# Kernel tuning notes

Measured on AMD Instinct MI355X. Metric: run time of the kernel, lower is better.

## Reference

```python
import jax, jax.numpy as jnp
import numpy as np

B, N, E, H = 32, 256, 768, 12
D = E // H
SCALING = D ** -0.5


def setup_inputs() -> dict:
    key = jax.random.key(0)
    ks = jax.random.split(key, 10)
    inp = {
        "query": jax.random.normal(ks[0], (B, N, E), dtype=jnp.float32),
        "attn_bias": jax.random.normal(ks[1], (B * H, N, N), dtype=jnp.float32),
        "delta_pos": jax.random.normal(ks[2], (B, N, N, 3), dtype=jnp.float32),
        # Linear params stored as (in, out) so y = x @ W + b (equivalent to torch Linear).
        "Wq": jax.random.normal(ks[3], (E, E), dtype=jnp.float32) * 0.02,
        "bq": jnp.zeros((E,), dtype=jnp.float32),
        "Wk": jax.random.normal(ks[4], (E, E), dtype=jnp.float32) * 0.02,
        "bk": jnp.zeros((E,), dtype=jnp.float32),
        "Wv": jax.random.normal(ks[5], (E, E), dtype=jnp.float32) * 0.02,
        "bv": jnp.zeros((E,), dtype=jnp.float32),
        # force_proj: Linear(E, 1, bias=False) -> weight vector (E,)
        "wf": jax.random.normal(ks[6], (E,), dtype=jnp.float32) * 0.02,
    }
    return inp


def reference(query, attn_bias, delta_pos, Wq, bq, Wk, bk, Wv, bv, wf):
    b, n, e = query.shape
    h, d = H, D
    # QKV projections -> (b, n, h, d)
    q = (query @ Wq + bq).reshape(b, n, h, d) * SCALING
    k = (query @ Wk + bk).reshape(b, n, h, d)
    v = (query @ Wv + bv).reshape(b, n, h, d)
    # attention scores (b, h, n, n)
    attn = jnp.einsum("bnhd,bmhd->bhnm", q, k)
    # add bias on flattened (b*h, n, n), softmax over last dim (dropout=0.1 disabled: eval mode)
    probs = jax.nn.softmax(attn.reshape(b * h, n, n) + attn_bias, axis=-1)
    probs = probs.reshape(b, h, n, n)
    # equivariant weighted sum: x[b,n,c,h,d] = sum_m probs[b,h,n,m] * delta_pos[b,n,m,c] * v[b,m,h,d]
    x = jnp.einsum("bhnm,bnmc,bmhd->bnchd", probs, delta_pos, v)
    x = x.reshape(b, n, 3, e)
    # force projection (shared Linear(E,1,bias=False) applied per spatial component)
    force = jnp.einsum("bnce,e->bnc", x, wf).astype(jnp.float32)
    return force
```

## Files before the change

### kernel.cpp

```cpp
#include <hip/hip_runtime.h>
#include <hip/hip_bf16.h>

#define Bc 32
#define Nc 256
#define Ec 768
#define Hc 12
#define Dc 64

typedef __attribute__((ext_vector_type(8))) __bf16 bf16x8;
typedef __attribute__((ext_vector_type(8))) unsigned short u16x8;
typedef __attribute__((ext_vector_type(4))) float f32x4;

__device__ __forceinline__ unsigned short f2bf(float x) {
  union { float f; unsigned u; } v; v.f = x;
  unsigned r = v.u + 0x7fff + ((v.u >> 16) & 1);
  return (unsigned short)(r >> 16);
}

#define GL2LDS(gp, lp) __builtin_amdgcn_global_load_lds( \
    (__attribute__((address_space(1))) void*)(gp),        \
    (__attribute__((address_space(3))) void*)(lp), 16, 0, 0)

__global__ __launch_bounds__(256) void k_trans(const float* __restrict__ Wq,
                                               const float* __restrict__ Wk,
                                               unsigned short* __restrict__ WT) {
  __shared__ float tile[32][33];
  const float* W = blockIdx.z ? Wk : Wq;
  float scale = blockIdx.z ? 1.0f : 0.125f;
  int rowoff = blockIdx.z ? Ec : 0;
  int k0 = blockIdx.x * 32, n0 = blockIdx.y * 32;
  int r = threadIdx.x >> 5, c = threadIdx.x & 31;
  #pragma unroll
  for (int it = 0; it < 4; ++it)
    tile[r + 8 * it][c] = W[(k0 + r + 8 * it) * Ec + n0 + c];
  __syncthreads();
  #pragma unroll
  for (int it = 0; it < 4; ++it)
    WT[(rowoff + n0 + r + 8 * it) * Ec + k0 + c] = f2bf(scale * tile[c][r + 8 * it]);
}

__global__ void k_build_wvf(const float* __restrict__ Wv, const float* __restrict__ bv,
                            const float* __restrict__ wf,
                            const float* __restrict__ bq, const float* __restrict__ bk,
                            float* __restrict__ Wvf, float* __restrict__ bvf,
                            float* __restrict__ bb) {
  int idx = blockIdx.x * 256 + threadIdx.x;
  if (idx < Ec * Hc) {
    int e = idx / Hc, h = idx % Hc;
    float s = 0.f;
    for (int d = 0; d < Dc; ++d) s += Wv[e * Ec + h * Dc + d] * wf[h * Dc + d];
    Wvf[idx] = s;
  }
  if (idx < Hc) {
    float s = 0.f;
    for (int d = 0; d < Dc; ++d) s += bv[idx * Dc + d] * wf[idx * Dc + d];
    bvf[idx] = s;
  }
  if (idx < 2 * Ec)
    bb[idx] = (idx < Ec) ? 0.125f * bq[idx] : bk[idx - Ec];
}

__global__ __launch_bounds__(256) void k_vf(const float* __restrict__ query,
                                            const float* __restrict__ Wvf,
                                            const float* __restrict__ bvf,
                                            float* __restrict__ vfT,
                                            unsigned short* __restrict__ Xb) {
  __shared__ float wl[Ec * 13];
  __shared__ float bl[Hc];
  for (int i = threadIdx.x; i < Ec * Hc; i += 256) {
    int e = i / Hc, h = i % Hc;
    wl[e * 13 + h] = Wvf[i];
  }
  if (threadIdx.x < Hc) bl[threadIdx.x] = bvf[threadIdx.x];
  __syncthreads();
  int warp = threadIdx.x >> 6, lane = threadIdx.x & 63;
  int r = blockIdx.x * 4 + warp;
  float q[12];
  #pragma unroll
  for (int i = 0; i < 12; ++i) q[i] = query[r * Ec + lane + 64 * i];
  #pragma unroll
  for (int i = 0; i < 12; ++i) Xb[r * Ec + lane + 64 * i] = f2bf(q[i]);
  int b = r >> 8, m = r & 255;
  for (int h = 0; h < Hc; ++h) {
    float s = 0.f;
    #pragma unroll
    for (int i = 0; i < 12; ++i) s += q[i] * wl[(lane + 64 * i) * 13 + h];
    #pragma unroll
    for (int off = 32; off; off >>= 1) s += __shfl_xor(s, off);
    if (lane == 0) vfT[(b * Hc + h) * Nc + m] = s + bl[h];
  }
}

__global__ __launch_bounds__(256) void k_gemm_qk(const unsigned short* __restrict__ Xb,
                                                 const unsigned short* __restrict__ WT,
                                                 const float* __restrict__ bb,
                                                 unsigned short* __restrict__ QK) {
  __shared__ unsigned short As[128 * 64];
  __shared__ unsigned short Bs[128 * 64];
  int bm = blockIdx.x, bn = blockIdx.y;
  int t = threadIdx.x;
  int wave = t >> 6, lane = t & 63;
  int wr = wave >> 1, wc = wave & 1;
  int lrow = lane & 15, lq = lane >> 4;
  const int row0 = bm * 128, col0 = bn * 128;

  int srow = wave * 8 + (lane >> 3);
  int soct = (lane & 7);

  f32x4 acc[4][4];
  #pragma unroll
  for (int m = 0; m < 4; ++m)
    #pragma unroll
    for (int n = 0; n < 4; ++n) acc[m][n] = f32x4{0.f, 0.f, 0.f, 0.f};

  for (int ks = 0; ks < Ec; ks += 64) {
    #pragma unroll
    for (int i = 0; i < 4; ++i) {
      int r = i * 32 + srow;
      int go = soct ^ (r & 7);
      GL2LDS(Xb + (row0 + r) * Ec + ks + go * 8, As + i * 2048 + wave * 512);
      GL2LDS(WT + (col0 + r) * Ec + ks + go * 8, Bs + i * 2048 + wave * 512);
    }
    __syncthreads();
    bf16x8 af[4][2], bfg[4][2];
    #pragma unroll
    for (int m = 0; m < 4; ++m) {
      int ra = wr * 64 + m * 16 + lrow;
      #pragma unroll
      for (int kk = 0; kk < 2; ++kk) {
        int o = kk * 4 + lq;
        af[m][kk] = *(const bf16x8*)(As + ra * 64 + ((o ^ (ra & 7)) << 3));
      }
    }
    #pragma unroll
    for (int n = 0; n < 4; ++n) {
      int rb = wc * 64 + n * 16 + lrow;
      #pragma unroll
      for (int kk = 0; kk < 2; ++kk) {
        int o = kk * 4 + lq;
        bfg[n][kk] = *(const bf16x8*)(Bs + rb * 64 + ((o ^ (rb & 7)) << 3));
      }
    }
    #pragma unroll
    for (int kk = 0; kk < 2; ++kk)
      #pragma unroll
      for (int m = 0; m < 4; ++m)
        #pragma unroll
        for (int n = 0; n < 4; ++n)
          acc[m][n] = __builtin_amdgcn_mfma_f32_16x16x32_bf16(af[m][kk], bfg[n][kk], acc[m][n], 0, 0, 0);
    __syncthreads();
  }
  int crow = lq * 4, ccol = lane & 15;
  #pragma unroll
  for (int m = 0; m < 4; ++m)
    #pragma unroll
    for (int n = 0; n < 4; ++n) {
      int col = col0 + wc * 64 + n * 16 + ccol;
      float bias = bb[col];
      #pragma unroll
      for (int j = 0; j < 4; ++j) {
        int row = row0 + wr * 64 + m * 16 + crow + j;
        QK[row * 1536 + col] = f2bf(acc[m][n][j] + bias);
      }
    }
}

__global__ __launch_bounds__(256, 4) void k_attn(const unsigned short* __restrict__ QK,
                                                 const float* __restrict__ bias,
                                                 const float* __restrict__ vfT,
                                                 const float* __restrict__ delta,
                                                 float* __restrict__ fpart) {
  __shared__ float S[16 * 256];
  __shared__ float vfl[6][256];

  int bi = blockIdx.x;
  int xcd = bi & 7, slot = bi >> 3;
  int b = xcd * 4 + (slot >> 5);
  int rem = slot & 31;
  int nt = rem >> 1, hg = rem & 1;
  int n0 = nt * 16;

  int t = threadIdx.x, w = t >> 6, l = t & 63;
  int lq = l >> 4, lr = l & 15;

  #pragma unroll
  for (int i = 0; i < 6; ++i)
    vfl[i][t] = vfT[(b * Hc + hg * 6 + i) * Nc + t];

  float w_reg[4][4];
  #pragma unroll
  for (int p = 0; p < 4; ++p)
    #pragma unroll
    for (int i = 0; i < 4; ++i) w_reg[p][i] = 0.f;

  const unsigned short* Qbase = QK + (size_t)b * Nc * 1536;
  const unsigned short* Kbase = Qbase + 768;

  for (int hh = 0; hh < 6; ++hh) {
    int h = hg * 6 + hh;
    float4 bias4[4];
    const float* bp = bias + (size_t)(b * Hc + h) * Nc * Nc;
    #pragma unroll
    for (int p = 0; p < 4; ++p)
      bias4[p] = *(const float4*)(bp + (n0 + w * 4 + p) * Nc + l * 4);
    bf16x8 qf[2];
    #pragma unroll
    for (int kk = 0; kk < 2; ++kk)
      qf[kk] = *(const bf16x8*)(Qbase + (n0 + lr) * 1536 + h * 64 + kk * 32 + lq * 8);
    f32x4 acc[4];
    #pragma unroll
    for (int mf = 0; mf < 4; ++mf) acc[mf] = f32x4{0.f, 0.f, 0.f, 0.f};
    #pragma unroll
    for (int mf = 0; mf < 4; ++mf)
      #pragma unroll
      for (int kk = 0; kk < 2; ++kk) {
        bf16x8 af = *(const bf16x8*)(Kbase + (w * 64 + mf * 16 + lr) * 1536 + h * 64 + kk * 32 + lq * 8);
        acc[mf] = __builtin_amdgcn_mfma_f32_16x16x32_bf16(af, qf[kk], acc[mf], 0, 0, 0);
      }
    #pragma unroll
    for (int mf = 0; mf < 4; ++mf) {
      int m0 = w * 64 + mf * 16 + lq * 4;
      *(f32x4*)&S[lr * 256 + (m0 ^ ((lr & 7) << 2))] = acc[mf];
    }
    __syncthreads();
    #pragma unroll
    for (int p = 0; p < 4; ++p) {
      int r = w * 4 + p;
      float4 sv = *(const float4*)&S[r * 256 + ((l * 4) ^ ((r & 7) << 2))];
      float p0 = __expf(sv.x + bias4[p].x);
      float p1 = __expf(sv.y + bias4[p].y);
      float p2 = __expf(sv.z + bias4[p].z);
      float p3 = __expf(sv.w + bias4[p].w);
      float ssum = (p0 + p1) + (p2 + p3);
      #pragma unroll
      for (int off = 1; off < 64; off <<= 1) ssum += __shfl_xor(ssum, off);
      float inv = 1.f / ssum;
      float4 vf4 = *(const float4*)&vfl[hh][l * 4];
      w_reg[p][0] += p0 * inv * vf4.x;
      w_reg[p][1] += p1 * inv * vf4.y;
      w_reg[p][2] += p2 * inv * vf4.z;
      w_reg[p][3] += p3 * inv * vf4.w;
    }
    __syncthreads();
  }
  #pragma unroll
  for (int p = 0; p < 4; ++p) {
    int r = w * 4 + p, n = n0 + r;
    const float* dp = delta + ((size_t)(b * Nc + n) * Nc + l * 4) * 3;
    float4 d0 = *(const float4*)(dp);
    float4 d1 = *(const float4*)(dp + 4);
    float4 d2 = *(const float4*)(dp + 8);
    float w0 = w_reg[p][0], w1 = w_reg[p][1], w2 = w_reg[p][2], w3 = w_reg[p][3];
    float f0 = w0 * d0.x + w1 * d0.w + w2 * d1.z + w3 * d2.y;
    float f1 = w0 * d0.y + w1 * d1.x + w2 * d1.w + w3 * d2.z;
    float f2 = w0 * d0.z + w1 * d1.y + w2 * d2.x + w3 * d2.w;
    #pragma unroll
    for (int off = 1; off < 64; off <<= 1) {
      f0 += __shfl_xor(f0, off);
      f1 += __shfl_xor(f1, off);
      f2 += __shfl_xor(f2, off);
    }
    if (l == 0) {
      float4 v; v.x = f0; v.y = f1; v.z = f2; v.w = 0.f;
      *(float4*)(fpart + ((size_t)(hg * Bc + b) * Nc + n) * 4) = v;
    }
  }
}

__global__ __launch_bounds__(256) void k_force(const float* __restrict__ fpart,
                                               float* __restrict__ out) {
  int b = blockIdx.x, n = threadIdx.x;
  float4 a = *(const float4*)(fpart + ((size_t)(b)*Nc + n) * 4);
  float4 c = *(const float4*)(fpart + ((size_t)(Bc + b) * Nc + n) * 4);
  float* o = out + (size_t)(b * Nc + n) * 3;
  o[0] = a.x + c.x; o[1] = a.y + c.y; o[2] = a.z + c.z;
}

extern "C" void kernel_launch(void* const* d_in, const int* in_sizes, int n_in,
                              void* d_out, int out_size, void* d_ws, size_t ws_size,
                              hipStream_t stream) {
  const float* query = (const float*)d_in[0];
  const float* attn_bias = (const float*)d_in[1];
  const float* delta_pos = (const float*)d_in[2];
  const float* Wq = (const float*)d_in[3];
  const float* bq = (const float*)d_in[4];
  const float* Wk = (const float*)d_in[5];
  const float* bk = (const float*)d_in[6];
  const float* Wv = (const float*)d_in[7];
  const float* bv = (const float*)d_in[8];
  const float* wf = (const float*)d_in[9];
  float* out = (float*)d_out;

  char* ws = (char*)d_ws;
  unsigned short* WT  = (unsigned short*)(ws);
  unsigned short* QKb = (unsigned short*)(ws + 2359296);
  unsigned short* Xb  = (unsigned short*)(ws + 27525120);
  float* fpart = (float*)(ws + 27525120);
  float* vfT = (float*)(ws + 40108032);
  float* Wvf = (float*)(ws + 40501248);
  float* bvf = (float*)(ws + 40538112);
  float* bb  = (float*)(ws + 40538160);

  k_trans<<<dim3(24, 24, 2), 256, 0, stream>>>(Wq, Wk, WT);
  k_build_wvf<<<36, 256, 0, stream>>>(Wv, bv, wf, bq, bk, Wvf, bvf, bb);
  k_vf<<<2048, 256, 0, stream>>>(query, Wvf, bvf, vfT, Xb);
  k_gemm_qk<<<dim3(64, 12), 256, 0, stream>>>(Xb, WT, bb, QKb);
  k_attn<<<1024, 256, 0, stream>>>(QKb, attn_bias, vfT, delta_pos, fpart);
  k_force<<<Bc, 256, 0, stream>>>(fpart, out);
}
```

Measured before the change: 111.3 us.

## Software-pipeline per-head loads in attention kernel and remap GEMM blocks across XCDs

The attention kernel now prefetches the next head's K, Q, bias and vf values into registers while computing the current head. It double-buffers the score tile in shared memory so one barrier per head is removed, and drops the occupancy hint of 4 from its launch bounds. The QK GEMM launch is flattened to a 1D grid and remapped so consecutive blocks on the same XCD share tiles, for better L2 locality. This hides global load latency at the cost of higher register pressure, which may lower occupancy.

```diff
diff --git a/kernel.cpp b/kernel.cpp
--- a/kernel.cpp
+++ b/kernel.cpp
@@ -97,7 +97,8 @@
                                                  unsigned short* __restrict__ QK) {
   __shared__ unsigned short As[128 * 64];
   __shared__ unsigned short Bs[128 * 64];
-  int bm = blockIdx.x, bn = blockIdx.y;
+  int wgid = (blockIdx.x & 7) * 96 + (blockIdx.x >> 3);
+  int bm = wgid & 63, bn = wgid >> 6;
   int t = threadIdx.x;
   int wave = t >> 6, lane = t & 63;
   int wr = wave >> 1, wc = wave & 1;
@@ -165,13 +166,12 @@
     }
 }
 
-__global__ __launch_bounds__(256, 4) void k_attn(const unsigned short* __restrict__ QK,
-                                                 const float* __restrict__ bias,
-                                                 const float* __restrict__ vfT,
-                                                 const float* __restrict__ delta,
-                                                 float* __restrict__ fpart) {
-  __shared__ float S[16 * 256];
-  __shared__ float vfl[6][256];
+__global__ __launch_bounds__(256) void k_attn(const unsigned short* __restrict__ QK,
+                                              const float* __restrict__ bias,
+                                              const float* __restrict__ vfT,
+                                              const float* __restrict__ delta,
+                                              float* __restrict__ fpart) {
+  __shared__ float S[2][16 * 256];
 
   int bi = blockIdx.x;
   int xcd = bi & 7, slot = bi >> 3;
@@ -179,14 +179,11 @@
   int rem = slot & 31;
   int nt = rem >> 1, hg = rem & 1;
   int n0 = nt * 16;
+  int h0 = hg * 6;
 
   int t = threadIdx.x, w = t >> 6, l = t & 63;
   int lq = l >> 4, lr = l & 15;
 
-  #pragma unroll
-  for (int i = 0; i < 6; ++i)
-    vfl[i][t] = vfT[(b * Hc + hg * 6 + i) * Nc + t];
-
   float w_reg[4][4];
   #pragma unroll
   for (int p = 0; p < 4; ++p)
@@ -196,52 +193,89 @@
   const unsigned short* Qbase = QK + (size_t)b * Nc * 1536;
   const unsigned short* Kbase = Qbase + 768;
 
+  bf16x8 kc[4][2], qc[2];
+  float4 bc[4], vc;
+  {
+    int h = h0;
+    #pragma unroll
+    for (int kk = 0; kk < 2; ++kk)
+      qc[kk] = *(const bf16x8*)(Qbase + (n0 + lr) * 1536 + h * 64 + kk * 32 + lq * 8);
+    #pragma unroll
+    for (int mf = 0; mf < 4; ++mf)
+      #pragma unroll
+      for (int kk = 0; kk < 2; ++kk)
+        kc[mf][kk] = *(const bf16x8*)(Kbase + (w * 64 + mf * 16 + lr) * 1536 + h * 64 + kk * 32 + lq * 8);
+    const float* bp = bias + (size_t)(b * Hc + h) * Nc * Nc;
+    #pragma unroll
+    for (int p = 0; p < 4; ++p)
+      bc[p] = *(const float4*)(bp + (n0 + w * 4 + p) * Nc + l * 4);
+    vc = *(const float4*)(vfT + (size_t)(b * Hc + h) * Nc + l * 4);
+  }
+
+  #pragma unroll 1
   for (int hh = 0; hh < 6; ++hh) {
-    int h = hg * 6 + hh;
-    float4 bias4[4];
-    const float* bp = bias + (size_t)(b * Hc + h) * Nc * Nc;
-    #pragma unroll
-    for (int p = 0; p < 4; ++p)
-      bias4[p] = *(const float4*)(bp + (n0 + w * 4 + p) * Nc + l * 4);
-    bf16x8 qf[2];
-    #pragma unroll
-    for (int kk = 0; kk < 2; ++kk)
-      qf[kk] = *(const bf16x8*)(Qbase + (n0 + lr) * 1536 + h * 64 + kk * 32 + lq * 8);
     f32x4 acc[4];
     #pragma unroll
     for (int mf = 0; mf < 4; ++mf) acc[mf] = f32x4{0.f, 0.f, 0.f, 0.f};
     #pragma unroll
     for (int mf = 0; mf < 4; ++mf)
       #pragma unroll
-      for (int kk = 0; kk < 2; ++kk) {
-        bf16x8 af = *(const bf16x8*)(Kbase + (w * 64 + mf * 16 + lr) * 1536 + h * 64 + kk * 32 + lq * 8);
-        acc[mf] = __builtin_amdgcn_mfma_f32_16x16x32_bf16(af, qf[kk], acc[mf], 0, 0, 0);
-      }
+      for (int kk = 0; kk < 2; ++kk)
+        acc[mf] = __builtin_amdgcn_mfma_f32_16x16x32_bf16(kc[mf][kk], qc[kk], acc[mf], 0, 0, 0);
     #pragma unroll
     for (int mf = 0; mf < 4; ++mf) {
       int m0 = w * 64 + mf * 16 + lq * 4;
-      *(f32x4*)&S[lr * 256 + (m0 ^ ((lr & 7) << 2))] = acc[mf];
-    }
-    __syncthreads();
+      *(f32x4*)&S[hh & 1][lr * 256 + (m0 ^ ((lr & 7) << 2))] = acc[mf];
+    }
+    asm volatile("s_waitcnt lgkmcnt(0)" ::: "memory");
+    __builtin_amdgcn_sched_barrier(0);
+    __builtin_amdgcn_s_barrier();
+    bf16x8 kn[4][2], qn[2];
+    float4 bn[4], vn;
+    if (hh < 5) {
+      int h = h0 + hh + 1;
+      #pragma unroll
+      for (int kk = 0; kk < 2; ++kk)
+        qn[kk] = *(const bf16x8*)(Qbase + (n0 + lr) * 1536 + h * 64 + kk * 32 + lq * 8);
+      #pragma unroll
+      for (int mf = 0; mf < 4; ++mf)
+        #pragma unroll
+        for (int kk = 0; kk < 2; ++kk)
+          kn[mf][kk] = *(const bf16x8*)(Kbase + (w * 64 + mf * 16 + lr) * 1536 + h * 64 + kk * 32 + lq * 8);
+      const float* bp = bias + (size_t)(b * Hc + h) * Nc * Nc;
+      #pragma unroll
+      for (int p = 0; p < 4; ++p)
+        bn[p] = *(const float4*)(bp + (n0 + w * 4 + p) * Nc + l * 4);
+      vn = *(const float4*)(vfT + (size_t)(b * Hc + h) * Nc + l * 4);
+    }
+    __builtin_amdgcn_sched_barrier(0);
     #pragma unroll
     for (int p = 0; p < 4; ++p) {
       int r = w * 4 + p;
-      float4 sv = *(const float4*)&S[r * 256 + ((l * 4) ^ ((r & 7) << 2))];
-      float p0 = __expf(sv.x + bias4[p].x);
-      float p1 = __expf(sv.y + bias4[p].y);
-      float p2 = __expf(sv.z + bias4[p].z);
-      float p3 = __expf(sv.w + bias4[p].w);
+      float4 sv = *(const float4*)&S[hh & 1][r * 256 + ((l * 4) ^ ((r & 7) << 2))];
+      float p0 = __expf(sv.x + bc[p].x);
+      float p1 = __expf(sv.y + bc[p].y);
+      float p2 = __expf(sv.z + bc[p].z);
+      float p3 = __expf(sv.w + bc[p].w);
       float ssum = (p0 + p1) + (p2 + p3);
       #pragma unroll
       for (int off = 1; off < 64; off <<= 1) ssum += __shfl_xor(ssum, off);
       float inv = 1.f / ssum;
-      float4 vf4 = *(const float4*)&vfl[hh][l * 4];
-      w_reg[p][0] += p0 * inv * vf4.x;
-      w_reg[p][1] += p1 * inv * vf4.y;
-      w_reg[p][2] += p2 * inv * vf4.z;
-      w_reg[p][3] += p3 * inv * vf4.w;
-    }
-    __syncthreads();
+      w_reg[p][0] += p0 * inv * vc.x;
+      w_reg[p][1] += p1 * inv * vc.y;
+      w_reg[p][2] += p2 * inv * vc.z;
+      w_reg[p][3] += p3 * inv * vc.w;
+    }
+    if (hh < 5) {
+      #pragma unroll
+      for (int mf = 0; mf < 4; ++mf)
+        #pragma unroll
+        for (int kk = 0; kk < 2; ++kk) kc[mf][kk] = kn[mf][kk];
+      qc[0] = qn[0]; qc[1] = qn[1];
+      #pragma unroll
+      for (int p = 0; p < 4; ++p) bc[p] = bn[p];
+      vc = vn;
+    }
   }
   #pragma unroll
   for (int p = 0; p < 4; ++p) {
@@ -304,7 +338,7 @@
   k_trans<<<dim3(24, 24, 2), 256, 0, stream>>>(Wq, Wk, WT);
   k_build_wvf<<<36, 256, 0, stream>>>(Wv, bv, wf, bq, bk, Wvf, bvf, bb);
   k_vf<<<2048, 256, 0, stream>>>(query, Wvf, bvf, vfT, Xb);
-  k_gemm_qk<<<dim3(64, 12), 256, 0, stream>>>(Xb, WT, bb, QKb);
+  k_gemm_qk<<<768, 256, 0, stream>>>(Xb, WT, bb, QKb);
   k_attn<<<1024, 256, 0, stream>>>(QKb, attn_bias, vfT, delta_pos, fpart);
   k_force<<<Bc, 256, 0, stream>>>(fpart, out);
 }
```

After: 145.1 us. +30.3%, slower.
